# Performance work log

Hardware: AMD Instinct MI355X
Metric: run time of the kernel (lower is better)

## Reference

```python
import jax, jax.numpy as jnp
import numpy as np

N, C, H, W = 128, 3, 256, 256


def setup_inputs() -> dict:
    key = jax.random.key(0)
    k1, k2 = jax.random.split(key)
    inputs = jax.random.normal(k1, (N, C, H, W), dtype=jnp.float32)
    u = jax.random.uniform(k2, (N, 4), dtype=jnp.float32)
    # realistic crop params: scales in (0.3, 1.0], translations in (-0.2, 0.2)
    whbias = jnp.concatenate([0.3 + 0.7 * u[:, :2], 0.4 * u[:, 2:] - 0.2], axis=1)
    return {"inputs": inputs, "whbias": whbias}


def _reflect_clip(x, size):
    # PyTorch grid_sample padding_mode='reflection', align_corners=False:
    # reflect unnormalized coords about [-0.5, size-0.5], then clip to [0, size-1]
    span = float(size)
    x = jnp.abs(x + 0.5) % (2.0 * span)
    x = jnp.where(x > span, 2.0 * span - x, x) - 0.5
    return jnp.clip(x, 0.0, size - 1.0)


def _resized_crop(inputs, whbias):
    n, c, h, w = inputs.shape
    dt = inputs.dtype
    # F.affine_grid base coords, align_corners=False: centers of pixels in [-1, 1]
    xs = (jnp.arange(w, dtype=dt) + 0.5) * (2.0 / w) - 1.0  # [W]
    ys = (jnp.arange(h, dtype=dt) + 0.5) * (2.0 / h) - 1.0  # [H]
    w_s, h_s, w_b, h_b = whbias[:, 0], whbias[:, 1], whbias[:, 2], whbias[:, 3]
    # theta is diagonal + translation -> grid separable in x and y
    gx = w_s[:, None, None] * xs[None, None, :] + w_b[:, None, None]  # [N,H,W]
    gy = h_s[:, None, None] * ys[None, :, None] + h_b[:, None, None]  # [N,H,W]
    # unnormalize (align_corners=False): ix = ((gx+1)*W - 1)/2
    ix = _reflect_clip(((gx + 1.0) * w - 1.0) * 0.5, w)
    iy = _reflect_clip(((gy + 1.0) * h - 1.0) * 0.5, h)
    ix0 = jnp.floor(ix)
    iy0 = jnp.floor(iy)
    wx = (ix - ix0)[:, None]  # [N,1,H,W]
    wy = (iy - iy0)[:, None]
    ix0i = jnp.clip(ix0.astype(jnp.int32), 0, w - 1)
    ix1i = jnp.clip(ix0i + 1, 0, w - 1)
    iy0i = jnp.clip(iy0.astype(jnp.int32), 0, h - 1)
    iy1i = jnp.clip(iy0i + 1, 0, h - 1)

    def gather(img, yy, xx):  # img [C,H,W], yy/xx [H,W] -> [C,H,W]
        return img[:, yy, xx]

    g = jax.vmap(gather)
    v00 = g(inputs, iy0i, ix0i)
    v01 = g(inputs, iy0i, ix1i)
    v10 = g(inputs, iy1i, ix0i)
    v11 = g(inputs, iy1i, ix1i)
    # bilinear blend
    return (v00 * (1.0 - wx) * (1.0 - wy) + v01 * wx * (1.0 - wy)
            + v10 * (1.0 - wx) * wy + v11 * wx * wy)


def reference(inputs, whbias):
    # size=None -> no adaptive_avg_pool2d; output is [N,C,H,W]
    return _resized_crop(inputs, whbias)
```

## Files before the change

### kernel.cpp

```cpp
#include <hip/hip_runtime.h>


constexpr int N_ = 128, C_ = 3, H_ = 256, W_ = 256, HW_ = H_ * W_;
constexpr int ROWS_ = 5;
constexpr int LDSF_ = C_ * ROWS_ * W_ + 4;

typedef float f32x4 __attribute__((ext_vector_type(4)));

__device__ __forceinline__ void coord(float scale, float bias, float xf, int size,
                                      int& i0, int& i1, float& w) {
    const float span = (float)size;
    const float two  = 2.0f * span;
    float xs  = (xf + 0.5f) * (2.0f / span) - 1.0f;
    float g   = scale * xs + bias;
    float pre = ((g + 1.0f) * span - 1.0f) * 0.5f;
    float t = fabsf(pre + 0.5f);
    t = t - two * floorf(t * (1.0f / two));
    t = (t > span) ? (two - t) : t;
    t -= 0.5f;
    t = fminf(fmaxf(t, 0.0f), span - 1.0f);
    float f = floorf(t);
    w  = t - f;
    i0 = (int)f;
    i1 = min(i0 + 1, size - 1);
}

__global__ __launch_bounds__(256, 8)
void rrc_kernel(const float* __restrict__ in, const float* __restrict__ wh,
                float* __restrict__ out) {
    __shared__ float lds[LDSF_];
    const int n   = blockIdx.x >> 6;
    const int ys  = (blockIdx.x & 63) * 4;
    const int tid = threadIdx.x;
    const int xq  = tid & 63;
    const int yl  = tid >> 6;

    const float w_s = wh[n * 4 + 0];
    const float h_s = wh[n * 4 + 1];
    const float w_b = wh[n * 4 + 2];
    const float h_b = wh[n * 4 + 3];

    int rmin = H_ - 1, rmax = 0;
    int my0 = 0;  float wy = 0.0f;
#pragma unroll
    for (int r = 0; r < 4; ++r) {
        int a, b; float w;
        coord(h_s, h_b, (float)(ys + r), H_, a, b, w);
        rmin = min(rmin, a);
        rmax = max(rmax, b);
        if (r == yl) { my0 = a; wy = w; }
    }
    const int nrows = rmax - rmin + 1;

    const float* __restrict__ inN = in + (size_t)n * C_ * HW_;
#pragma unroll
    for (int c = 0; c < C_; ++c) {
        for (int r = yl; r < nrows; r += 4) {
            const f32x4 v = *reinterpret_cast<const f32x4*>(
                inN + c * HW_ + (rmin + r) * W_ + xq * 4);
            *reinterpret_cast<f32x4*>(&lds[(c * ROWS_ + r) * W_ + xq * 4]) = v;
        }
    }
    __syncthreads();

    int ix0[4]; float wx[4];
#pragma unroll
    for (int j = 0; j < 4; ++j) {
        int i1_unused;
        coord(w_s, w_b, (float)(xq * 4 + j), W_, ix0[j], i1_unused, wx[j]);
    }

    float* __restrict__ outN = out + (size_t)n * C_ * HW_;

    const int y  = ys + yl;
    const int b0 = (my0 - rmin) * W_;
    const int b1 = min(my0 + 1, H_ - 1) >= rmax ? (rmax - rmin) * W_
                                                : (my0 + 1 - rmin) * W_;
#pragma unroll
    for (int c = 0; c < C_; ++c) {
        const int co = c * ROWS_ * W_;
        f32x4 o;
#pragma unroll
        for (int j = 0; j < 4; ++j) {
            const int a0 = co + b0 + ix0[j];
            const int a1 = co + b1 + ix0[j];
            const float v00 = lds[a0];
            const float v01 = lds[a0 + 1];
            const float v10 = lds[a1];
            const float v11 = lds[a1 + 1];
            const float top = v00 + wx[j] * (v01 - v00);
            const float bot = v10 + wx[j] * (v11 - v10);
            o[j] = top + wy * (bot - top);
        }
        __builtin_nontemporal_store(o, reinterpret_cast<f32x4*>(
            outN + (c * H_ + y) * W_ + xq * 4));
    }
}

extern "C" void kernel_launch(void* const* d_in, const int* in_sizes, int n_in,
                              void* d_out, int out_size, void* d_ws, size_t ws_size,
                              hipStream_t stream) {
    const float* in = (const float*)d_in[0];
    const float* wh = (const float*)d_in[1];
    float* out      = (float*)d_out;
    (void)in_sizes; (void)n_in; (void)out_size; (void)d_ws; (void)ws_size;

    dim3 grid(N_ * 64);
    dim3 block(256);
    rrc_kernel<<<grid, block, 0, stream>>>(in, wh, out);
}
```

Measured before the change: 35.39 us.

## Split bilinear into separable horizontal then vertical passes through per-channel LDS

The kernel now interpolates each loaded source row horizontally once into a second LDS buffer, then forms output rows with vectorised vertical blends. Previously every output pixel did four scalar LDS gathers. It also shrinks LDS to one channel's rows plus the horizontal buffer, issues all global loads into registers up front, and drops the occupancy hint from launch bounds. The trade is two barriers per channel and extra LDS writes, plus horizontal work on all five rows even when fewer are needed.

```diff
diff --git a/kernel.cpp b/kernel.cpp
--- a/kernel.cpp
+++ b/kernel.cpp
@@ -3,12 +3,11 @@
 
 constexpr int N_ = 128, C_ = 3, H_ = 256, W_ = 256, HW_ = H_ * W_;
 constexpr int ROWS_ = 5;
-constexpr int LDSF_ = C_ * ROWS_ * W_ + 4;
 
 typedef float f32x4 __attribute__((ext_vector_type(4)));
 
 __device__ __forceinline__ void coord(float scale, float bias, float xf, int size,
-                                      int& i0, int& i1, float& w) {
+                                      int& i0, float& w) {
     const float span = (float)size;
     const float two  = 2.0f * span;
     float xs  = (xf + 0.5f) * (2.0f / span) - 1.0f;
@@ -22,13 +21,14 @@
     float f = floorf(t);
     w  = t - f;
     i0 = (int)f;
-    i1 = min(i0 + 1, size - 1);
 }
 
-__global__ __launch_bounds__(256, 8)
+__global__ __launch_bounds__(256)
 void rrc_kernel(const float* __restrict__ in, const float* __restrict__ wh,
                 float* __restrict__ out) {
-    __shared__ float lds[LDSF_];
+    __shared__ float raw[ROWS_ * W_ + 4];
+    __shared__ float Hl[ROWS_ * W_];
+
     const int n   = blockIdx.x >> 6;
     const int ys  = (blockIdx.x & 63) * 4;
     const int tid = threadIdx.x;
@@ -41,59 +41,56 @@
     const float h_b = wh[n * 4 + 3];
 
     int rmin = H_ - 1, rmax = 0;
-    int my0 = 0;  float wy = 0.0f;
+    int my0 = 0; float wy = 0.0f;
 #pragma unroll
     for (int r = 0; r < 4; ++r) {
-        int a, b; float w;
-        coord(h_s, h_b, (float)(ys + r), H_, a, b, w);
+        int a; float w;
+        coord(h_s, h_b, (float)(ys + r), H_, a, w);
         rmin = min(rmin, a);
-        rmax = max(rmax, b);
+        rmax = max(rmax, min(a + 1, H_ - 1));
         if (r == yl) { my0 = a; wy = w; }
     }
     const int nrows = rmax - rmin + 1;
+    const int words = nrows * 64;
+    const int b0 = (my0 - rmin) * W_;
+    const int b1 = (min(my0 + 1, H_ - 1) - rmin) * W_;
 
     const float* __restrict__ inN = in + (size_t)n * C_ * HW_;
+    const int r0 = tid >> 6,          sx0 = (tid & 63) * 4;
+    const int r1 = (tid + 256) >> 6,  sx1 = sx0;
+    const bool m1 = (tid + 256) < words;
+    const bool m0 = tid < words;
+    f32x4 ga[C_], gb[C_];
 #pragma unroll
     for (int c = 0; c < C_; ++c) {
-        for (int r = yl; r < nrows; r += 4) {
-            const f32x4 v = *reinterpret_cast<const f32x4*>(
-                inN + c * HW_ + (rmin + r) * W_ + xq * 4);
-            *reinterpret_cast<f32x4*>(&lds[(c * ROWS_ + r) * W_ + xq * 4]) = v;
-        }
+        if (m0) ga[c] = *reinterpret_cast<const f32x4*>(
+            inN + c * HW_ + (rmin + r0) * W_ + sx0);
+        if (m1) gb[c] = *reinterpret_cast<const f32x4*>(
+            inN + c * HW_ + (rmin + r1) * W_ + sx1);
     }
-    __syncthreads();
 
-    int ix0[4]; float wx[4];
-#pragma unroll
-    for (int j = 0; j < 4; ++j) {
-        int i1_unused;
-        coord(w_s, w_b, (float)(xq * 4 + j), W_, ix0[j], i1_unused, wx[j]);
-    }
+    int hix; float hwx;
+    coord(w_s, w_b, (float)tid, W_, hix, hwx);
 
     float* __restrict__ outN = out + (size_t)n * C_ * HW_;
 
-    const int y  = ys + yl;
-    const int b0 = (my0 - rmin) * W_;
-    const int b1 = min(my0 + 1, H_ - 1) >= rmax ? (rmax - rmin) * W_
-                                                : (my0 + 1 - rmin) * W_;
 #pragma unroll
     for (int c = 0; c < C_; ++c) {
-        const int co = c * ROWS_ * W_;
-        f32x4 o;
+        if (m0) *reinterpret_cast<f32x4*>(&raw[r0 * W_ + sx0]) = ga[c];
+        if (m1) *reinterpret_cast<f32x4*>(&raw[r1 * W_ + sx1]) = gb[c];
+        __syncthreads();
 #pragma unroll
-        for (int j = 0; j < 4; ++j) {
-            const int a0 = co + b0 + ix0[j];
-            const int a1 = co + b1 + ix0[j];
-            const float v00 = lds[a0];
-            const float v01 = lds[a0 + 1];
-            const float v10 = lds[a1];
-            const float v11 = lds[a1 + 1];
-            const float top = v00 + wx[j] * (v01 - v00);
-            const float bot = v10 + wx[j] * (v11 - v10);
-            o[j] = top + wy * (bot - top);
+        for (int k = 0; k < ROWS_; ++k) {
+            const float a = raw[k * W_ + hix];
+            const float b = raw[k * W_ + hix + 1];
+            Hl[k * W_ + tid] = a + hwx * (b - a);
         }
+        __syncthreads();
+        const f32x4 h0 = *reinterpret_cast<const f32x4*>(&Hl[b0 + xq * 4]);
+        const f32x4 h1 = *reinterpret_cast<const f32x4*>(&Hl[b1 + xq * 4]);
+        const f32x4 o  = h0 + wy * (h1 - h0);
         __builtin_nontemporal_store(o, reinterpret_cast<f32x4*>(
-            outN + (c * H_ + y) * W_ + xq * 4));
+            outN + (c * H_ + ys + yl) * W_ + xq * 4));
     }
 }
 
```

New measurement: 35.31 us. No clear change (-0.2%).
